# Optimization experiments

Hardware: AMD Instinct MI355X
Metric: run time of the kernel (lower is better)

The kernel has to match this reference:

```python
import jax, jax.numpy as jnp
import numpy as np

B, T, D, N = 16, 512, 1024, 16


def setup_inputs() -> dict:
    key = jax.random.key(0)
    ks = jax.random.split(key, 6)
    x = jax.random.normal(ks[0], (B, T, D), dtype=jnp.float32)
    h_tape_init = jax.random.normal(ks[1], (B, N, D), dtype=jnp.float32) * 0.1
    h_work_init = jnp.zeros((B, D), dtype=jnp.float32)
    W_h = jax.random.normal(ks[2], (D, D), dtype=jnp.float32) * 0.02
    W_xz = jax.random.normal(ks[3], (2 * D, D), dtype=jnp.float32) * 0.02
    b_h = jnp.zeros((D,), dtype=jnp.float32)
    W_write = jax.random.normal(ks[4], (D, D), dtype=jnp.float32) * 0.02
    return {"x": x, "h_tape_init": h_tape_init, "h_work_init": h_work_init,
            "W_h": W_h, "W_xz": W_xz, "b_h": b_h, "W_write": W_write}


def _e29a_scan(x, h_tape_init, h_work_init, W_h, W_xz, b_h, W_write):
    d = W_h.shape[0]
    scale = 1.0 / (d ** 0.5)
    xz = jnp.einsum('btd,ed->bte', x, W_xz)          # [B,T,2D]
    x_proj = xz[:, :, :d]                             # [B,T,D]
    z = xz[:, :, d:]                                  # [B,T,D]

    def step(carry, inp):
        h_tape, h_work = carry                        # [B,N,D], [B,D]
        x_proj_t, z_t = inp                           # [B,D], [B,D]
        read_scores = jnp.einsum('bd,bnd->bn', h_work, h_tape) * scale
        read_attn = jax.nn.softmax(read_scores, axis=-1)
        read_val = jnp.einsum('bn,bnd->bd', read_attn, h_tape)
        h_work_new = jnp.tanh(x_proj_t + h_work @ W_h.T + read_val + b_h)
        write_val = h_work_new @ W_write.T            # [B,D]
        write_scores = jnp.einsum('bd,bnd->bn', write_val, h_tape) * scale
        write_attn = jax.nn.softmax(write_scores, axis=-1)
        wa = write_attn[:, :, None]                   # [B,N,1]
        h_tape_new = h_tape * (1.0 - wa) + write_val[:, None, :] * wa
        gate = jax.nn.silu(z_t + read_val + h_work_new)
        output = h_work_new * gate
        return (h_tape_new, h_work_new), output

    inputs = (jnp.swapaxes(x_proj, 0, 1), jnp.swapaxes(z, 0, 1))  # [T,B,D]
    (h_tape_final, _), out_t = jax.lax.scan(step, (h_tape_init, h_work_init), inputs)
    output_all = jnp.swapaxes(out_t, 0, 1)            # [B,T,D]
    return output_all, h_tape_final


def reference(x, h_tape_init, h_work_init, W_h, W_xz, b_h, W_write):
    return _e29a_scan(x, h_tape_init, h_work_init, W_h, W_xz, b_h, W_write)
```

## Files before the change

kernel.cpp:

```cpp
#include <hip/hip_runtime.h>

typedef _Float16 half8 __attribute__((ext_vector_type(8)));
typedef _Float16 half4_t __attribute__((ext_vector_type(4)));
typedef _Float16 half2_t __attribute__((ext_vector_type(2)));
typedef float f32x4 __attribute__((ext_vector_type(4)));
typedef float f32x2 __attribute__((ext_vector_type(2)));
typedef unsigned long long u64;
typedef unsigned int u32;

#define SCALE 0.03125f

#define XZ_OFF   0ULL
#define RING_OFF 33554432ULL
#define XBF_OFF  33554432ULL
#define WXZ_OFF  50331648ULL
#define WH_OFF   54525952ULL
#define WW_OFF   56623104ULL
#define VOTE_OFF 58720256ULL
#define SEN_OFF  58724352ULL

#define SLOTB 36864ULL
#define R_WVP 0
#define R_H   32768

union Pk2 { u64 u[2]; half8 h8; };
union Pk1 { u64 u; half4_t h; };

__device__ __forceinline__ u64 ldq(const u64* p, bool mall) {
    return mall ? __hip_atomic_load(p, __ATOMIC_RELAXED, __HIP_MEMORY_SCOPE_AGENT) : *p;
}
__device__ __forceinline__ void stq(u64* p, u64 v, bool mall) {
    if (mall) __hip_atomic_store(p, v, __ATOMIC_RELAXED, __HIP_MEMORY_SCOPE_AGENT); else *p = v;
}
__device__ __forceinline__ u32 ldsen(u32* p) {
    return __hip_atomic_load(p, __ATOMIC_RELAXED, __HIP_MEMORY_SCOPE_AGENT);
}

#define FDOT(a,b,acc) acc = __builtin_amdgcn_fdot2((a),(b),(acc),false)
__device__ __forceinline__ half2_t hp2(half8 v, int i) {
    half2_t r; r[0] = v[2*i]; r[1] = v[2*i+1]; return r;
}

__global__ void cvt_kernel(const float* __restrict__ in, _Float16* __restrict__ o, int n4) {
    int i = blockIdx.x * 256 + threadIdx.x;
    if (i < n4) {
        f32x4 v = ((const f32x4*)in)[i];
        half4_t h;
        h[0] = (_Float16)v[0]; h[1] = (_Float16)v[1];
        h[2] = (_Float16)v[2]; h[3] = (_Float16)v[3];
        ((half4_t*)o)[i] = h;
    }
}

__launch_bounds__(256, 1)
__global__ void gemm_xz(const _Float16* __restrict__ A,
                        const _Float16* __restrict__ Bw,
                        _Float16* __restrict__ C) {
    __shared__ _Float16 As[128 * 40];
    __shared__ _Float16 Bs[128 * 40];
    const int tid = threadIdx.x;
    const int m0 = blockIdx.y * 128, n0 = blockIdx.x * 128;
    const int w = tid >> 6, lane = tid & 63;
    const int mw = (w >> 1) * 64, nw = (w & 1) * 64;
    const int row = lane & 15, q = lane >> 4;
    f32x4 acc[4][4];
    #pragma unroll
    for (int mt = 0; mt < 4; mt++)
        #pragma unroll
        for (int nt = 0; nt < 4; nt++)
            acc[mt][nt] = (f32x4){0.f, 0.f, 0.f, 0.f};

    for (int k0 = 0; k0 < 1024; k0 += 32) {
        __syncthreads();
        for (int cc = tid; cc < 512; cc += 256) {
            int r = cc >> 2, kc = (cc & 3) * 8;
            *(half8*)(&As[r * 40 + kc]) = *(const half8*)(&A[(size_t)(m0 + r) * 1024 + k0 + kc]);
            *(half8*)(&Bs[r * 40 + kc]) = *(const half8*)(&Bw[(size_t)(n0 + r) * 1024 + k0 + kc]);
        }
        __syncthreads();
        half8 af[4], bf[4];
        #pragma unroll
        for (int mt = 0; mt < 4; mt++) af[mt] = *(const half8*)(&As[(mw + mt * 16 + row) * 40 + q * 8]);
        #pragma unroll
        for (int nt = 0; nt < 4; nt++) bf[nt] = *(const half8*)(&Bs[(nw + nt * 16 + row) * 40 + q * 8]);
        #pragma unroll
        for (int mt = 0; mt < 4; mt++)
            #pragma unroll
            for (int nt = 0; nt < 4; nt++)
                acc[mt][nt] = __builtin_amdgcn_mfma_f32_16x16x32_f16(af[mt], bf[nt], acc[mt][nt], 0, 0, 0);
    }
    #pragma unroll
    for (int mt = 0; mt < 4; mt++)
        #pragma unroll
        for (int nt = 0; nt < 4; nt++)
            #pragma unroll
            for (int r = 0; r < 4; r++) {
                int gm = m0 + mw + mt * 16 + q * 4 + r;
                int gn = n0 + nw + nt * 16 + row;
                C[(size_t)gm * 2048 + gn] = (_Float16)acc[mt][nt][r];
            }
}

__launch_bounds__(256, 1)
__global__ void scan_kernel(const _Float16* __restrict__ xz,
                            const float* __restrict__ tape_in,
                            const float* __restrict__ h_in,
                            const float* __restrict__ bh,
                            const _Float16* __restrict__ wh,
                            const _Float16* __restrict__ ww,
                            char* ring,
                            u32* sen,
                            u32* vote,
                            float* __restrict__ out) {
    const int bx = blockIdx.x;
    const int g = (bx & 7) * 2 + ((bx >> 3) & 1);
    const int s = bx >> 4;
    const int tid = threadIdx.x;
    const int lane = tid & 63;
    const int nn = tid >> 4, c16 = tid & 15;
    const int cc = tid >> 2, q = tid & 3;

    __shared__ __align__(16) _Float16 h_prev[1024];
    __shared__ __align__(16) _Float16 h_own[64];
    __shared__ __align__(16) float rv_l[1024];
    __shared__ float p_l[256 * 17];
    __shared__ float sc_l[16];
    __shared__ float pad_l[15000];
    __shared__ int sh_same;

    { volatile float* vp = pad_l; vp[tid] = 0.f; }

    if (tid == 0) {
        u32 xcc;
        asm volatile("s_getreg_b32 %0, hwreg(HW_REG_XCC_ID)" : "=s"(xcc));
        xcc &= 7u;
        __hip_atomic_store(&vote[bx * 4], xcc + 1u, __ATOMIC_RELAXED, __HIP_MEMORY_SCOPE_AGENT);
        int same = 1; u32 ref = 0;
        for (int m = 0; m < 16; m++) {
            int mb = m * 16 + ((g & 1) << 3) + (g >> 1);
            u32 v; int spin = 0;
            while ((v = __hip_atomic_load(&vote[mb * 4], __ATOMIC_RELAXED, __HIP_MEMORY_SCOPE_AGENT)) == 0u) {
                if (++spin > 1000000) { v = 0xFFFFFFFFu; break; }
                __builtin_amdgcn_s_sleep(2);
            }
            if (m == 0) ref = v;
            if (v != ref || v == 0xFFFFFFFFu) same = 0;
        }
        sh_same = same;
    }
    __syncthreads();
    const bool mall = (sh_same == 0);
    bool dead = false;

    const int qx = q << 1;
    half8 whr[32];
    {
        const _Float16* wp = wh + (size_t)(s * 64 + cc) * 1024 + q * 256;
        #pragma unroll
        for (int jj = 0; jj < 32; jj++)
            whr[jj] = *(const half8*)(wp + ((jj ^ qx) * 8));
    }
    half8 wwr[4][8];
    {
        const _Float16* wp = ww + (size_t)(tid * 4) * 1024 + s * 64;
        #pragma unroll
        for (int jj = 0; jj < 4; jj++)
            #pragma unroll
            for (int kk = 0; kk < 8; kk++)
                wwr[jj][kk] = *(const half8*)(wp + jj * 1024 + kk * 8);
    }
    f32x4 tp[16];
    #pragma unroll
    for (int n = 0; n < 16; n++)
        tp[n] = *(const f32x4*)(&tape_in[(size_t)(g * 16 + n) * 1024 + tid * 4]);
    const float bhc = bh[s * 64 + cc];

    {
        f32x4 h4 = *(const f32x4*)(&h_in[(size_t)g * 1024 + tid * 4]);
        half4_t hh;
        hh[0] = (_Float16)h4[0]; hh[1] = (_Float16)h4[1];
        hh[2] = (_Float16)h4[2]; hh[3] = (_Float16)h4[3];
        *(half4_t*)(&h_prev[tid * 4]) = hh;
    }
    __syncthreads();

    u32* cnt = sen + (size_t)g * 32;

    for (int t = 0; t <= 512; t++) {
        char* srd  = ring + (size_t)(g * 8 + ((t + 7) & 7)) * SLOTB;
        char* spub = ring + (size_t)(g * 8 + (t & 7)) * SLOTB;
        const bool havew = (t >= 1);
        float xp = 0.f, zz = 0.f;
        if (t < 512) {
            size_t m = (size_t)(g * 512 + t) * 2048 + s * 64 + cc;
            xp = (float)xz[m];
            zz = (float)xz[m + 1024];
        }
        f32x4 wv4 = (f32x4){0.f, 0.f, 0.f, 0.f};
        if (havew) {
            if (!dead && lane == 0) {
                int spin = 0;
                while (ldsen(cnt) < (u32)(16 * t)) {
                    if (++spin > 2000000) { dead = true; break; }
                    __builtin_amdgcn_s_sleep(1);
                }
            }
            asm volatile("" ::: "memory");
            if (tid < 128) {
                const u64* Hp = (const u64*)(srd + R_H);
                Pk2 u;
                u.u[0] = ldq(&Hp[tid * 2], mall);
                u.u[1] = ldq(&Hp[tid * 2 + 1], mall);
                *(half8*)(&h_prev[tid * 8]) = u.h8;
            }
            const u64* Wp = (const u64*)(srd + R_WVP);
            #pragma unroll
            for (int sl = 0; sl < 16; sl++) {
                Pk1 u; u.u = ldq(&Wp[sl * 256 + tid], mall);
                wv4[0] += (float)u.h[0]; wv4[1] += (float)u.h[1];
                wv4[2] += (float)u.h[2]; wv4[3] += (float)u.h[3];
            }
            {
                float p[16];
                #pragma unroll
                for (int n = 0; n < 16; n++) {
                    f32x4 d = tp[n];
                    p[n] = wv4[0]*d[0] + wv4[1]*d[1] + wv4[2]*d[2] + wv4[3]*d[3];
                }
                #pragma unroll
                for (int n = 0; n < 16; n++) p_l[tid * 17 + n] = p[n];
            }
            __syncthreads();
            {
                float scw = 0.f;
                #pragma unroll
                for (int m2 = 0; m2 < 16; m2++) scw += p_l[(c16 + 16 * m2) * 17 + nn];
                #pragma unroll
                for (int d2 = 1; d2 < 16; d2 <<= 1) scw += __shfl_xor(scw, d2, 16);
                if (c16 == 0) sc_l[nn] = scw;
            }
            __syncthreads();
            {
                float e[16], mxw = -1e30f;
                #pragma unroll
                for (int n = 0; n < 16; n++) { e[n] = sc_l[n] * SCALE; mxw = fmaxf(mxw, e[n]); }
                float smw = 0.f;
                #pragma unroll
                for (int n = 0; n < 16; n++) { e[n] = __expf(e[n] - mxw); smw += e[n]; }
                float invw = 1.f / smw;
                #pragma unroll
                for (int n = 0; n < 16; n++) {
                    float wan = e[n] * invw;
                    f32x4 d = tp[n];
                    d[0] += wan * (wv4[0] - d[0]);
                    d[1] += wan * (wv4[1] - d[1]);
                    d[2] += wan * (wv4[2] - d[2]);
                    d[3] += wan * (wv4[3] - d[3]);
                    tp[n] = d;
                }
            }
        }
        if (t == 512) break;

        {
            half4_t hh = *(const half4_t*)(&h_prev[tid * 4]);
            float h0 = (float)hh[0], h1 = (float)hh[1], h2 = (float)hh[2], h3 = (float)hh[3];
            float p[16];
            #pragma unroll
            for (int n = 0; n < 16; n++) {
                f32x4 d = tp[n];
                p[n] = h0*d[0] + h1*d[1] + h2*d[2] + h3*d[3];
            }
            #pragma unroll
            for (int n = 0; n < 16; n++) p_l[tid * 17 + n] = p[n];
        }
        __syncthreads();
        float sc = 0.f;
        #pragma unroll
        for (int m2 = 0; m2 < 16; m2++) sc += p_l[(c16 + 16 * m2) * 17 + nn];
        #pragma unroll
        for (int d2 = 1; d2 < 16; d2 <<= 1) sc += __shfl_xor(sc, d2, 16);
        if (c16 == 0) sc_l[nn] = sc;
        __syncthreads();
        float r[16], mx = -1e30f;
        #pragma unroll
        for (int n = 0; n < 16; n++) { r[n] = sc_l[n] * SCALE; mx = fmaxf(mx, r[n]); }
        float sm = 0.f;
        #pragma unroll
        for (int n = 0; n < 16; n++) { r[n] = __expf(r[n] - mx); sm += r[n]; }
        float inv = 1.f / sm;
        f32x4 rv4 = (f32x4){0.f, 0.f, 0.f, 0.f};
        #pragma unroll
        for (int n = 0; n < 16; n++) rv4 += (r[n] * inv) * tp[n];
        *(f32x4*)(&rv_l[tid * 4]) = rv4;
        float a0 = 0.f, a1 = 0.f, a2 = 0.f, a3 = 0.f;
        #pragma unroll
        for (int jj = 0; jj < 32; jj++) {
            half8 hp8 = *(const half8*)(&h_prev[q * 256 + ((jj ^ qx) * 8)]);
            half8 wc = whr[jj];
            FDOT(hp2(wc,0), hp2(hp8,0), a0);
            FDOT(hp2(wc,1), hp2(hp8,1), a1);
            FDOT(hp2(wc,2), hp2(hp8,2), a2);
            FDOT(hp2(wc,3), hp2(hp8,3), a3);
        }
        float av = (a0 + a1) + (a2 + a3);
        av += __shfl_xor(av, 1);
        av += __shfl_xor(av, 2);
        __syncthreads();
        float rd = rv_l[s * 64 + cc];
        float hv = tanhf(av + xp + rd + bhc);
        float g2 = zz + rd + hv;
        float o = hv * g2 / (1.f + __expf(-g2));
        if (q == 0) h_own[cc] = (_Float16)hv;
        __syncthreads();
        half8 hr[8];
        #pragma unroll
        for (int kk = 0; kk < 8; kk++) hr[kk] = *(const half8*)(&h_own[kk * 8]);
        float w0 = 0.f, w1 = 0.f, w2 = 0.f, w3 = 0.f;
        #pragma unroll
        for (int kk = 0; kk < 8; kk++) {
            half8 h8 = hr[kk];
            #pragma unroll
            for (int pp = 0; pp < 4; pp++) {
                FDOT(hp2(wwr[0][kk],pp), hp2(h8,pp), w0);
                FDOT(hp2(wwr[1][kk],pp), hp2(h8,pp), w1);
                FDOT(hp2(wwr[2][kk],pp), hp2(h8,pp), w2);
                FDOT(hp2(wwr[3][kk],pp), hp2(h8,pp), w3);
            }
        }
        {
            Pk1 wq;
            wq.h = (half4_t){(_Float16)w0, (_Float16)w1, (_Float16)w2, (_Float16)w3};
            stq(&((u64*)(spub + R_WVP))[s * 256 + tid], wq.u, mall);
            if (tid < 8) {
                Pk2 u; u.h8 = *(const half8*)(&h_own[tid * 8]);
                u64* Hp = (u64*)(spub + R_H);
                stq(&Hp[s * 16 + tid * 2],     u.u[0], mall);
                stq(&Hp[s * 16 + tid * 2 + 1], u.u[1], mall);
            }
        }
        __syncthreads();
        if (tid == 0)
            __hip_atomic_fetch_add(cnt, 1u, __ATOMIC_RELAXED, __HIP_MEMORY_SCOPE_AGENT);
        if (q == 0) out[(size_t)(g * 512 + t) * 1024 + s * 64 + cc] = o;
    }
    if (s == 0) {
        #pragma unroll
        for (int n = 0; n < 16; n++)
            *(f32x4*)(&out[8388608ULL + (size_t)(g * 16 + n) * 1024 + tid * 4]) = tp[n];
    }
}

extern "C" void kernel_launch(void* const* d_in, const int* in_sizes, int n_in,
                              void* d_out, int out_size, void* d_ws, size_t ws_size,
                              hipStream_t stream) {
    const float* x     = (const float*)d_in[0];
    const float* tape0 = (const float*)d_in[1];
    const float* h0    = (const float*)d_in[2];
    const float* Wh    = (const float*)d_in[3];
    const float* Wxz   = (const float*)d_in[4];
    const float* bh    = (const float*)d_in[5];
    const float* Ww    = (const float*)d_in[6];

    char* ws = (char*)d_ws;
    _Float16* xbf   = (_Float16*)(ws + XBF_OFF);
    _Float16* wxzbf = (_Float16*)(ws + WXZ_OFF);
    _Float16* whbf  = (_Float16*)(ws + WH_OFF);
    _Float16* wwbf  = (_Float16*)(ws + WW_OFF);
    _Float16* xzbf  = (_Float16*)(ws + XZ_OFF);
    char* ring      = ws + RING_OFF;
    u32* vote       = (u32*)(ws + VOTE_OFF);
    u32* sen        = (u32*)(ws + SEN_OFF);

    hipMemsetAsync(ws + VOTE_OFF, 0, 4096 + 32768, stream);

    cvt_kernel<<<8192, 256, 0, stream>>>(x, xbf, 2097152);
    cvt_kernel<<<2048, 256, 0, stream>>>(Wxz, wxzbf, 524288);
    cvt_kernel<<<1024, 256, 0, stream>>>(Wh, whbf, 262144);
    cvt_kernel<<<1024, 256, 0, stream>>>(Ww, wwbf, 262144);

    gemm_xz<<<dim3(16, 64), 256, 0, stream>>>(xbf, wxzbf, xzbf);

    scan_kernel<<<256, 256, 0, stream>>>(xzbf, tape0, h0, bh, whbf, wwbf,
                                         ring, sen, vote, (float*)d_out);
}
```

Baseline: 3.042 ms.

## Double scan block threads and replace shared atomic counter with per-block step flags

The persistent scan kernel goes from 256 to 512 threads per block. Per-thread register work (W_h slice, W_write rows, tape columns) is halved, and the reductions gain an extra shuffle stage. The single atomic counter that all 16 blocks of a group incremented each step is replaced by per-block sequence words; 16 lanes poll them in parallel, which removes atomic contention on one address. The cost is more waves per step, taking part in barriers and LDS traffic, and smaller 32-bit ring stores.

New measurement: 2.703 ms. -11.2%, faster.

```diff
diff --git a/kernel.cpp b/kernel.cpp
--- a/kernel.cpp
+++ b/kernel.cpp
@@ -24,7 +24,7 @@
 #define R_H   32768
 
 union Pk2 { u64 u[2]; half8 h8; };
-union Pk1 { u64 u; half4_t h; };
+union PkW { u32 u; half2_t h; };
 
 __device__ __forceinline__ u64 ldq(const u64* p, bool mall) {
     return mall ? __hip_atomic_load(p, __ATOMIC_RELAXED, __HIP_MEMORY_SCOPE_AGENT) : *p;
@@ -32,8 +32,17 @@
 __device__ __forceinline__ void stq(u64* p, u64 v, bool mall) {
     if (mall) __hip_atomic_store(p, v, __ATOMIC_RELAXED, __HIP_MEMORY_SCOPE_AGENT); else *p = v;
 }
+__device__ __forceinline__ u32 ldw(const u32* p, bool mall) {
+    return mall ? __hip_atomic_load(p, __ATOMIC_RELAXED, __HIP_MEMORY_SCOPE_AGENT) : *p;
+}
+__device__ __forceinline__ void stw(u32* p, u32 v, bool mall) {
+    if (mall) __hip_atomic_store(p, v, __ATOMIC_RELAXED, __HIP_MEMORY_SCOPE_AGENT); else *p = v;
+}
 __device__ __forceinline__ u32 ldsen(u32* p) {
     return __hip_atomic_load(p, __ATOMIC_RELAXED, __HIP_MEMORY_SCOPE_AGENT);
+}
+__device__ __forceinline__ void stsen(u32* p, u32 v) {
+    __hip_atomic_store(p, v, __ATOMIC_RELAXED, __HIP_MEMORY_SCOPE_AGENT);
 }
 
 #define FDOT(a,b,acc) acc = __builtin_amdgcn_fdot2((a),(b),(acc),false)
@@ -101,7 +110,7 @@
             }
 }
 
-__launch_bounds__(256, 1)
+__launch_bounds__(512, 1)
 __global__ void scan_kernel(const _Float16* __restrict__ xz,
                             const float* __restrict__ tape_in,
                             const float* __restrict__ h_in,
@@ -117,15 +126,15 @@
     const int s = bx >> 4;
     const int tid = threadIdx.x;
     const int lane = tid & 63;
-    const int nn = tid >> 4, c16 = tid & 15;
-    const int cc = tid >> 2, q = tid & 3;
+    const int cc = tid >> 3, q = tid & 7;
+    const int nn = tid >> 5, c32 = tid & 31;
 
     __shared__ __align__(16) _Float16 h_prev[1024];
     __shared__ __align__(16) _Float16 h_own[64];
     __shared__ __align__(16) float rv_l[1024];
-    __shared__ float p_l[256 * 17];
+    __shared__ float p_l[512 * 17];
     __shared__ float sc_l[16];
-    __shared__ float pad_l[15000];
+    __shared__ float pad_l[10000];
     __shared__ int sh_same;
 
     { volatile float* vp = pad_l; vp[tid] = 0.f; }
@@ -153,38 +162,37 @@
     bool dead = false;
 
     const int qx = q << 1;
-    half8 whr[32];
+    half8 whr[16];
     {
-        const _Float16* wp = wh + (size_t)(s * 64 + cc) * 1024 + q * 256;
-        #pragma unroll
-        for (int jj = 0; jj < 32; jj++)
-            whr[jj] = *(const half8*)(wp + ((jj ^ qx) * 8));
-    }
-    half8 wwr[4][8];
+        const _Float16* wp = wh + (size_t)(s * 64 + cc) * 1024 + q * 128;
+        #pragma unroll
+        for (int jj = 0; jj < 16; jj++)
+            whr[jj] = *(const half8*)(wp + (((jj ^ qx) & 15) * 8));
+    }
+    half8 wwr[2][8];
     {
-        const _Float16* wp = ww + (size_t)(tid * 4) * 1024 + s * 64;
-        #pragma unroll
-        for (int jj = 0; jj < 4; jj++)
+        const _Float16* wp = ww + (size_t)(tid * 2) * 1024 + s * 64;
+        #pragma unroll
+        for (int jj = 0; jj < 2; jj++)
             #pragma unroll
             for (int kk = 0; kk < 8; kk++)
                 wwr[jj][kk] = *(const half8*)(wp + jj * 1024 + kk * 8);
     }
-    f32x4 tp[16];
+    f32x2 tp[16];
     #pragma unroll
     for (int n = 0; n < 16; n++)
-        tp[n] = *(const f32x4*)(&tape_in[(size_t)(g * 16 + n) * 1024 + tid * 4]);
+        tp[n] = *(const f32x2*)(&tape_in[(size_t)(g * 16 + n) * 1024 + tid * 2]);
     const float bhc = bh[s * 64 + cc];
 
     {
-        f32x4 h4 = *(const f32x4*)(&h_in[(size_t)g * 1024 + tid * 4]);
-        half4_t hh;
-        hh[0] = (_Float16)h4[0]; hh[1] = (_Float16)h4[1];
-        hh[2] = (_Float16)h4[2]; hh[3] = (_Float16)h4[3];
-        *(half4_t*)(&h_prev[tid * 4]) = hh;
+        f32x2 h2 = *(const f32x2*)(&h_in[(size_t)g * 1024 + tid * 2]);
+        half2_t hh; hh[0] = (_Float16)h2[0]; hh[1] = (_Float16)h2[1];
+        *(half2_t*)(&h_prev[tid * 2]) = hh;
     }
     __syncthreads();
 
-    u32* cnt = sen + (size_t)g * 32;
+    u32* senrow = sen + (size_t)(g * 16 + s) * 32;
+    const int senb = g * 16;
 
     for (int t = 0; t <= 512; t++) {
         char* srd  = ring + (size_t)(g * 8 + ((t + 7) & 7)) * SLOTB;
@@ -196,11 +204,11 @@
             xp = (float)xz[m];
             zz = (float)xz[m + 1024];
         }
-        f32x4 wv4 = (f32x4){0.f, 0.f, 0.f, 0.f};
+        f32x2 wv2 = (f32x2){0.f, 0.f};
         if (havew) {
-            if (!dead && lane == 0) {
+            if (!dead && lane < 16) {
                 int spin = 0;
-                while (ldsen(cnt) < (u32)(16 * t)) {
+                while (ldsen(&sen[(size_t)(senb + lane) * 32]) < (u32)t) {
                     if (++spin > 2000000) { dead = true; break; }
                     __builtin_amdgcn_s_sleep(1);
                 }
@@ -213,19 +221,18 @@
                 u.u[1] = ldq(&Hp[tid * 2 + 1], mall);
                 *(half8*)(&h_prev[tid * 8]) = u.h8;
             }
-            const u64* Wp = (const u64*)(srd + R_WVP);
+            const u32* Wp = (const u32*)(srd + R_WVP);
             #pragma unroll
             for (int sl = 0; sl < 16; sl++) {
-                Pk1 u; u.u = ldq(&Wp[sl * 256 + tid], mall);
-                wv4[0] += (float)u.h[0]; wv4[1] += (float)u.h[1];
-                wv4[2] += (float)u.h[2]; wv4[3] += (float)u.h[3];
+                PkW u; u.u = ldw(&Wp[sl * 512 + tid], mall);
+                wv2[0] += (float)u.h[0]; wv2[1] += (float)u.h[1];
             }
             {
                 float p[16];
                 #pragma unroll
                 for (int n = 0; n < 16; n++) {
-                    f32x4 d = tp[n];
-                    p[n] = wv4[0]*d[0] + wv4[1]*d[1] + wv4[2]*d[2] + wv4[3]*d[3];
+                    f32x2 d = tp[n];
+                    p[n] = wv2[0]*d[0] + wv2[1]*d[1];
                 }
                 #pragma unroll
                 for (int n = 0; n < 16; n++) p_l[tid * 17 + n] = p[n];
@@ -234,10 +241,10 @@
             {
                 float scw = 0.f;
                 #pragma unroll
-                for (int m2 = 0; m2 < 16; m2++) scw += p_l[(c16 + 16 * m2) * 17 + nn];
-                #pragma unroll
-                for (int d2 = 1; d2 < 16; d2 <<= 1) scw += __shfl_xor(scw, d2, 16);
-                if (c16 == 0) sc_l[nn] = scw;
+                for (int m2 = 0; m2 < 16; m2++) scw += p_l[(c32 + 32 * m2) * 17 + nn];
+                #pragma unroll
+                for (int d2 = 1; d2 < 32; d2 <<= 1) scw += __shfl_xor(scw, d2, 32);
+                if (c32 == 0) sc_l[nn] = scw;
             }
             __syncthreads();
             {
@@ -251,11 +258,9 @@
                 #pragma unroll
                 for (int n = 0; n < 16; n++) {
                     float wan = e[n] * invw;
-                    f32x4 d = tp[n];
-                    d[0] += wan * (wv4[0] - d[0]);
-                    d[1] += wan * (wv4[1] - d[1]);
-                    d[2] += wan * (wv4[2] - d[2]);
-                    d[3] += wan * (wv4[3] - d[3]);
+                    f32x2 d = tp[n];
+                    d[0] += wan * (wv2[0] - d[0]);
+                    d[1] += wan * (wv2[1] - d[1]);
                     tp[n] = d;
                 }
             }
@@ -263,13 +268,13 @@
         if (t == 512) break;
 
         {
-            half4_t hh = *(const half4_t*)(&h_prev[tid * 4]);
-            float h0 = (float)hh[0], h1 = (float)hh[1], h2 = (float)hh[2], h3 = (float)hh[3];
+            half2_t hh = *(const half2_t*)(&h_prev[tid * 2]);
+            float h0 = (float)hh[0], h1 = (float)hh[1];
             float p[16];
             #pragma unroll
             for (int n = 0; n < 16; n++) {
-                f32x4 d = tp[n];
-                p[n] = h0*d[0] + h1*d[1] + h2*d[2] + h3*d[3];
+                f32x2 d = tp[n];
+                p[n] = h0*d[0] + h1*d[1];
             }
             #pragma unroll
             for (int n = 0; n < 16; n++) p_l[tid * 17 + n] = p[n];
@@ -277,10 +282,10 @@
         __syncthreads();
         float sc = 0.f;
         #pragma unroll
-        for (int m2 = 0; m2 < 16; m2++) sc += p_l[(c16 + 16 * m2) * 17 + nn];
-        #pragma unroll
-        for (int d2 = 1; d2 < 16; d2 <<= 1) sc += __shfl_xor(sc, d2, 16);
-        if (c16 == 0) sc_l[nn] = sc;
+        for (int m2 = 0; m2 < 16; m2++) sc += p_l[(c32 + 32 * m2) * 17 + nn];
+        #pragma unroll
+        for (int d2 = 1; d2 < 32; d2 <<= 1) sc += __shfl_xor(sc, d2, 32);
+        if (c32 == 0) sc_l[nn] = sc;
         __syncthreads();
         float r[16], mx = -1e30f;
         #pragma unroll
@@ -289,14 +294,18 @@
         #pragma unroll
         for (int n = 0; n < 16; n++) { r[n] = __expf(r[n] - mx); sm += r[n]; }
         float inv = 1.f / sm;
-        f32x4 rv4 = (f32x4){0.f, 0.f, 0.f, 0.f};
-        #pragma unroll
-        for (int n = 0; n < 16; n++) rv4 += (r[n] * inv) * tp[n];
-        *(f32x4*)(&rv_l[tid * 4]) = rv4;
+        f32x2 rv2 = (f32x2){0.f, 0.f};
+        #pragma unroll
+        for (int n = 0; n < 16; n++) {
+            float ra = r[n] * inv;
+            rv2[0] += ra * tp[n][0];
+            rv2[1] += ra * tp[n][1];
+        }
+        *(f32x2*)(&rv_l[tid * 2]) = rv2;
         float a0 = 0.f, a1 = 0.f, a2 = 0.f, a3 = 0.f;
         #pragma unroll
-        for (int jj = 0; jj < 32; jj++) {
-            half8 hp8 = *(const half8*)(&h_prev[q * 256 + ((jj ^ qx) * 8)]);
+        for (int jj = 0; jj < 16; jj++) {
+            half8 hp8 = *(const half8*)(&h_prev[q * 128 + (((jj ^ qx) & 15) * 8)]);
             half8 wc = whr[jj];
             FDOT(hp2(wc,0), hp2(hp8,0), a0);
             FDOT(hp2(wc,1), hp2(hp8,1), a1);
@@ -306,6 +315,7 @@
         float av = (a0 + a1) + (a2 + a3);
         av += __shfl_xor(av, 1);
         av += __shfl_xor(av, 2);
+        av += __shfl_xor(av, 4);
         __syncthreads();
         float rd = rv_l[s * 64 + cc];
         float hv = tanhf(av + xp + rd + bhc);
@@ -316,7 +326,7 @@
         half8 hr[8];
         #pragma unroll
         for (int kk = 0; kk < 8; kk++) hr[kk] = *(const half8*)(&h_own[kk * 8]);
-        float w0 = 0.f, w1 = 0.f, w2 = 0.f, w3 = 0.f;
+        float w0 = 0.f, w1 = 0.f;
         #pragma unroll
         for (int kk = 0; kk < 8; kk++) {
             half8 h8 = hr[kk];
@@ -324,14 +334,12 @@
             for (int pp = 0; pp < 4; pp++) {
                 FDOT(hp2(wwr[0][kk],pp), hp2(h8,pp), w0);
                 FDOT(hp2(wwr[1][kk],pp), hp2(h8,pp), w1);
-                FDOT(hp2(wwr[2][kk],pp), hp2(h8,pp), w2);
-                FDOT(hp2(wwr[3][kk],pp), hp2(h8,pp), w3);
             }
         }
         {
-            Pk1 wq;
-            wq.h = (half4_t){(_Float16)w0, (_Float16)w1, (_Float16)w2, (_Float16)w3};
-            stq(&((u64*)(spub + R_WVP))[s * 256 + tid], wq.u, mall);
+            PkW wq;
+            wq.h = (half2_t){(_Float16)w0, (_Float16)w1};
+            stw(&((u32*)(spub + R_WVP))[s * 512 + tid], wq.u, mall);
             if (tid < 8) {
                 Pk2 u; u.h8 = *(const half8*)(&h_own[tid * 8]);
                 u64* Hp = (u64*)(spub + R_H);
@@ -340,14 +348,13 @@
             }
         }
         __syncthreads();
-        if (tid == 0)
-            __hip_atomic_fetch_add(cnt, 1u, __ATOMIC_RELAXED, __HIP_MEMORY_SCOPE_AGENT);
+        if (tid == 0) stsen(senrow, (u32)(t + 1));
         if (q == 0) out[(size_t)(g * 512 + t) * 1024 + s * 64 + cc] = o;
     }
     if (s == 0) {
         #pragma unroll
         for (int n = 0; n < 16; n++)
-            *(f32x4*)(&out[8388608ULL + (size_t)(g * 16 + n) * 1024 + tid * 4]) = tp[n];
+            *(f32x2*)(&out[8388608ULL + (size_t)(g * 16 + n) * 1024 + tid * 2]) = tp[n];
     }
 }
 
@@ -381,6 +388,6 @@
 
     gemm_xz<<<dim3(16, 64), 256, 0, stream>>>(xbf, wxzbf, xzbf);
 
-    scan_kernel<<<256, 256, 0, stream>>>(xzbf, tape0, h0, bh, whbf, wwbf,
+    scan_kernel<<<256, 512, 0, stream>>>(xzbf, tape0, h0, bh, whbf, wwbf,
                                          ring, sen, vote, (float*)d_out);
 }
```
